# Optimization experiments

Hardware: AMD Instinct MI355X
Metric: run time of the kernel (lower is better)

Reference implementation:

```python
import jax, jax.numpy as jnp
import numpy as np

T, B, H = 256, 512, 2048

def setup_inputs() -> dict:
    key = jax.random.key(0)
    ks = jax.random.split(key, 10)
    s = 1.0 / np.sqrt(H)  # torch RNN/Linear init scale (values only need to be sane)
    return {
        "initial_input": jax.random.normal(ks[0], (B, 1), jnp.float32),
        "hidden": jax.random.normal(ks[1], (B, H), jnp.float32),
        "targets": jax.random.normal(ks[2], (T, B, 1), jnp.float32),
        "W_ih": jax.random.normal(ks[3], (H, 1), jnp.float32) * s,
        "b_ih": jax.random.normal(ks[4], (H,), jnp.float32) * s,
        "W_hh": jax.random.normal(ks[5], (H, H), jnp.float32) * s,
        "b_hh": jax.random.normal(ks[6], (H,), jnp.float32) * s,
        "W_out": jax.random.normal(ks[7], (1, H), jnp.float32) * s,
        "b_out": jax.random.normal(ks[8], (1,), jnp.float32) * s,
        "tf_mask": jax.random.randint(ks[9], (T,), 0, 2) > 0,  # per-step teacher-force decision
    }

def reference(initial_input, hidden, targets, W_ih, b_ih, W_hh, b_hh, W_out, b_out, tf_mask):
    def step(carry, xs):
        h, x = carry                      # h: [B,H], x: [B,1]
        tgt, tf = xs                      # tgt: [B,1], tf: scalar bool
        h = jnp.tanh(x @ W_ih.T + b_ih + h @ W_hh.T + b_hh)  # [B,H]
        y = h @ W_out.T + b_out           # [B,1]
        x_next = jnp.where(tf, tgt, y)
        return (h, x_next), y
    (_, _), outputs = jax.lax.scan(step, (hidden, initial_input), (targets, tf_mask))
    return outputs  # [T,B,1]
```

## Files before the change

kernel.cpp:

```cpp
#include <hip/hip_runtime.h>

using half8   = __attribute__((ext_vector_type(8))) _Float16;
using f32x16  = __attribute__((ext_vector_type(16))) float;
using float4v = __attribute__((ext_vector_type(4))) float;

#define T_STEPS 256
#define BATCH   512
#define HID     2048
#define KS      128

__device__ __forceinline__ f32x16 zero16() {
  f32x16 z;
#pragma unroll
  for (int r = 0; r < 16; ++r) z[r] = 0.0f;
  return z;
}

__device__ __forceinline__ half8 load16_sc0(const half8* p) {
  half8 r;
  asm volatile("global_load_dwordx4 %0, %1, off sc0" : "=v"(r) : "v"(p));
  return r;
}
__device__ __forceinline__ float load4_sc0(const float* p) {
  float r;
  asm volatile("global_load_dword %0, %1, off sc0" : "=v"(r) : "v"(p));
  return r;
}

__global__ void pack_whh_k(const float* __restrict__ whh, half8* __restrict__ bp) {
  int id   = blockIdx.x * 256 + threadIdx.x;
  int lane = id & 63;
  int ks   = (id >> 6) & 127;
  int nblk = id >> 13;
  int j = nblk * 32 + (lane & 31);
  int k = ks * 16 + (lane >> 5) * 8;
  const float4v* src = (const float4v*)(whh + (size_t)j * HID + k);
  float4v a = src[0], b = src[1];
  half8 v;
  v[0]=(_Float16)a[0]; v[1]=(_Float16)a[1]; v[2]=(_Float16)a[2]; v[3]=(_Float16)a[3];
  v[4]=(_Float16)b[0]; v[5]=(_Float16)b[1]; v[6]=(_Float16)b[2]; v[7]=(_Float16)b[3];
  bp[id] = v;
}

__global__ void pack_h_k(const float* __restrict__ hsrc, half8* __restrict__ hp) {
  int id   = blockIdx.x * 256 + threadIdx.x;
  int lane = id & 63;
  int ks   = (id >> 6) & 127;
  int bblk = id >> 13;
  int b = bblk * 32 + (lane & 31);
  int k = ks * 16 + (lane >> 5) * 8;
  const float4v* src = (const float4v*)(hsrc + (size_t)b * HID + k);
  float4v a = src[0], c = src[1];
  half8 v;
  v[0]=(_Float16)a[0]; v[1]=(_Float16)a[1]; v[2]=(_Float16)a[2]; v[3]=(_Float16)a[3];
  v[4]=(_Float16)c[0]; v[5]=(_Float16)c[1]; v[6]=(_Float16)c[2]; v[7]=(_Float16)c[3];
  hp[id] = v;
}

__global__ void bias_k(const float* __restrict__ bih, const float* __restrict__ bhh,
                       float* __restrict__ bias) {
  int i = blockIdx.x * 256 + threadIdx.x;
  if (i < HID) bias[i] = bih[i] + bhh[i];
}

__global__ void tf_expand_k(const int* __restrict__ tf, int* __restrict__ tfc,
                            unsigned* __restrict__ bar) {
  __shared__ int fmt;
  if (threadIdx.x == 0) {
    const unsigned* u = (const unsigned*)tf;
    int all01 = 1;
    for (int i = 0; i < 32; ++i) if (u[i] > 1u) all01 = 0;
    if (all01) {
      int odd0 = 1;
      for (int i = 1; i < 32; i += 2) if (u[i] != 0u) odd0 = 0;
      fmt = odd0 ? 2 : 1;
    } else fmt = 0;
  }
  __syncthreads();
  int i = threadIdx.x;
  int v;
  if (fmt == 2)      v = tf[2 * i];
  else if (fmt == 1) v = tf[i];
  else               v = (int)((const unsigned char*)tf)[i];
  tfc[i] = v ? 1 : 0;
  bar[i] = 0u;
}

__global__ __launch_bounds__(512) void rnn_persist(
    const float* __restrict__ x0,   const float* __restrict__ tgt,
    const int*   __restrict__ tfc,  const float* __restrict__ wih,
    const float* __restrict__ wout, const float* __restrict__ bias,
    const float* __restrict__ bout, const half8* __restrict__ wp,
    half8* __restrict__ h0,         half8* __restrict__ h1,
    float* __restrict__ ypg,        float* __restrict__ out,
    unsigned* __restrict__ bar) {
  __shared__ float part[4][64][68];
  __shared__ float hs[64][68];
  __shared__ float xs[64];
  __shared__ float ypart[8][64];
  __shared__ float wih_s[64], wout_s[64], bias_s[64];
  __shared__ int   tfs[T_STEPS];
  __shared__ int   mn_s[2];

  const int tid = threadIdx.x;
  const int w = tid >> 6;
  const int l = tid & 63;
  const int hi = l >> 5;
  const int c = l & 31;

  if (tid == 0) {
    unsigned xcc = __builtin_amdgcn_s_getreg((31 << 11) | (0 << 6) | 20) & 15u;
    unsigned x = xcc & 7u;
    unsigned r = __hip_atomic_fetch_add(&bar[x * 32 + 16], 1u, __ATOMIC_RELAXED,
                                        __HIP_MEMORY_SCOPE_AGENT);
    mn_s[0] = (int)x;
    mn_s[1] = (int)(r & 31u);
  }
  __syncthreads();
  const int m = mn_s[0];
  const int n = mn_s[1];
  const float bo = bout[0];

  if (tid < 64) {
    int j = n * 64 + tid;
    wih_s[tid]  = wih[j];
    wout_s[tid] = wout[j];
    bias_s[tid] = bias[j];
  }
  if (tid < T_STEPS) tfs[tid] = tfc[tid];

  half8 wb0[16], wb1[16];
  {
    const half8* b0p = wp + ((size_t)(2 * n + 0) * KS + w * 16) * 64 + l;
    const half8* b1p = wp + ((size_t)(2 * n + 1) * KS + w * 16) * 64 + l;
#pragma unroll
    for (int i = 0; i < 16; ++i) { wb0[i] = b0p[i * 64]; wb1[i] = b1p[i * 64]; }
  }
  __syncthreads();

  for (int t = 0; t < T_STEPS; ++t) {
    const half8* hr = (t & 1) ? h1 : h0;
    half8*       hw = (t & 1) ? h0 : h1;

    if (tid < 64) {
      float x;
      if (t == 0) {
        x = x0[m * 64 + tid];
      } else {
        const float* yp = ypg + ((size_t)((t - 1) & 1) * 8 + m) * 32 * 64 + tid;
        float a[32];
#pragma unroll
        for (int i = 0; i < 32; ++i) a[i] = load4_sc0(yp + i * 64);
        asm volatile("s_waitcnt vmcnt(0)" ::: "memory");
        __builtin_amdgcn_sched_barrier(0);
        float s = 0.0f;
#pragma unroll
        for (int i = 0; i < 32; ++i) s += a[i];
        float ysum = s + bo;
        if (n == 0) out[(size_t)(t - 1) * BATCH + m * 64 + tid] = ysum;
        x = tfs[t - 1] ? tgt[(size_t)(t - 1) * BATCH + m * 64 + tid] : ysum;
      }
      xs[tid] = x;
    }

    f32x16 acc00 = zero16(), acc01 = zero16(), acc10 = zero16(), acc11 = zero16();
    {
      const half8* a0p = hr + ((size_t)(2 * m + 0) * KS + w * 16) * 64 + l;
      const half8* a1p = hr + ((size_t)(2 * m + 1) * KS + w * 16) * 64 + l;
#pragma unroll
      for (int kk = 0; kk < 4; ++kk) {
        half8 a0[4], a1[4];
#pragma unroll
        for (int i = 0; i < 4; ++i) {
          a0[i] = load16_sc0(a0p + (kk * 4 + i) * 64);
          a1[i] = load16_sc0(a1p + (kk * 4 + i) * 64);
        }
        asm volatile("s_waitcnt vmcnt(0)" ::: "memory");
        __builtin_amdgcn_sched_barrier(0);
#pragma unroll
        for (int i = 0; i < 4; ++i) {
          acc00 = __builtin_amdgcn_mfma_f32_32x32x16_f16(a0[i], wb0[kk * 4 + i], acc00, 0, 0, 0);
          acc01 = __builtin_amdgcn_mfma_f32_32x32x16_f16(a0[i], wb1[kk * 4 + i], acc01, 0, 0, 0);
          acc10 = __builtin_amdgcn_mfma_f32_32x32x16_f16(a1[i], wb0[kk * 4 + i], acc10, 0, 0, 0);
          acc11 = __builtin_amdgcn_mfma_f32_32x32x16_f16(a1[i], wb1[kk * 4 + i], acc11, 0, 0, 0);
        }
      }
    }

    if (w < 4) {
#pragma unroll
      for (int r = 0; r < 16; ++r) {
        int row0 = (r & 3) + 8 * (r >> 2) + 4 * hi;
        part[w][row0     ][c     ] = acc00[r];
        part[w][row0     ][c + 32] = acc01[r];
        part[w][row0 + 32][c     ] = acc10[r];
        part[w][row0 + 32][c + 32] = acc11[r];
      }
    }
    __syncthreads();
    if (w >= 4) {
      int ww = w - 4;
#pragma unroll
      for (int r = 0; r < 16; ++r) {
        int row0 = (r & 3) + 8 * (r >> 2) + 4 * hi;
        part[ww][row0     ][c     ] += acc00[r];
        part[ww][row0     ][c + 32] += acc01[r];
        part[ww][row0 + 32][c     ] += acc10[r];
        part[ww][row0 + 32][c + 32] += acc11[r];
      }
    }
    __syncthreads();

    {
      int mb = w & 1, nb = (w >> 1) & 1, rh = w >> 2;
#pragma unroll
      for (int r = 0; r < 8; ++r) {
        int rr = rh * 8 + r;
        int row = mb * 32 + (rr & 3) + 8 * (rr >> 2) + 4 * hi;
        int col = nb * 32 + c;
        float s = part[0][row][col] + part[1][row][col]
                + part[2][row][col] + part[3][row][col];
        s += bias_s[col] + xs[row] * wih_s[col];
        hs[row][col] = tanhf(s);
      }
    }
    __syncthreads();

    {
      int row = tid & 63;
      int g   = tid >> 6;
      float hv[8];
      float4v v0 = *(const float4v*)&hs[row][g * 8];
      float4v v1 = *(const float4v*)&hs[row][g * 8 + 4];
      hv[0]=v0[0]; hv[1]=v0[1]; hv[2]=v0[2]; hv[3]=v0[3];
      hv[4]=v1[0]; hv[5]=v1[1]; hv[6]=v1[2]; hv[7]=v1[3];

      float yp = 0.0f;
#pragma unroll
      for (int e = 0; e < 8; ++e) yp += hv[e] * wout_s[g * 8 + e];
      ypart[g][row] = yp;

      half8 f;
#pragma unroll
      for (int e = 0; e < 8; ++e) f[e] = (_Float16)hv[e];
      int bblk = 2 * m + (row >> 5);
      int ksg  = n * 4 + (g >> 1);
      int lane = (g & 1) * 32 + (row & 31);
      hw[((size_t)bblk * KS + ksg) * 64 + lane] = f;
    }
    __syncthreads();

    if (w == 0) {
      float y = ypart[0][tid] + ypart[1][tid] + ypart[2][tid] + ypart[3][tid]
              + ypart[4][tid] + ypart[5][tid] + ypart[6][tid] + ypart[7][tid];
      ypg[(((size_t)(t & 1) * 8 + m) * 32 + n) * 64 + tid] = y;
      asm volatile("s_waitcnt vmcnt(0)" ::: "memory");
    }

    if (tid == 0) {
      __hip_atomic_fetch_add(&bar[m * 32], 1u, __ATOMIC_RELAXED,
                             __HIP_MEMORY_SCOPE_AGENT);
      unsigned tgt_cnt = 32u * (unsigned)(t + 1);
      while (__hip_atomic_load(&bar[m * 32], __ATOMIC_RELAXED,
                               __HIP_MEMORY_SCOPE_AGENT) < tgt_cnt)
        __builtin_amdgcn_s_sleep(1);
    }
    __syncthreads();
  }

  if (n == 0 && tid < 64) {
    const float* yp = ypg + ((size_t)((T_STEPS - 1) & 1) * 8 + m) * 32 * 64 + tid;
    float a[32];
#pragma unroll
    for (int i = 0; i < 32; ++i) a[i] = load4_sc0(yp + i * 64);
    asm volatile("s_waitcnt vmcnt(0)" ::: "memory");
    __builtin_amdgcn_sched_barrier(0);
    float s = 0.0f;
#pragma unroll
    for (int i = 0; i < 32; ++i) s += a[i];
    out[(size_t)(T_STEPS - 1) * BATCH + m * 64 + tid] = s + bo;
  }
}

extern "C" void kernel_launch(void* const* d_in, const int* in_sizes, int n_in,
                              void* d_out, int out_size, void* d_ws, size_t ws_size,
                              hipStream_t stream) {
  (void)in_sizes; (void)n_in; (void)out_size; (void)ws_size;
  const float* x0   = (const float*)d_in[0];
  const float* hid  = (const float*)d_in[1];
  const float* tgt  = (const float*)d_in[2];
  const float* wih  = (const float*)d_in[3];
  const float* bih  = (const float*)d_in[4];
  const float* whh  = (const float*)d_in[5];
  const float* bhh  = (const float*)d_in[6];
  const float* wout = (const float*)d_in[7];
  const float* bout = (const float*)d_in[8];
  const int*   tf   = (const int*)d_in[9];
  float* out = (float*)d_out;

  char* ws = (char*)d_ws;
  half8*    wp   = (half8*)ws;
  half8*    h0   = (half8*)(ws + (8u  << 20));
  half8*    h1   = (half8*)(ws + (10u << 20));
  float*    bias = (float*)(ws + (12u << 20));
  int*      tfc  = (int*)  (ws + (12u << 20) + 8192);
  unsigned* bar  = (unsigned*)(ws + (12u << 20) + 16384);
  float*    ypg  = (float*)(ws + (12u << 20) + 32768);

  pack_whh_k <<<2048, 256, 0, stream>>>(whh, wp);
  pack_h_k   <<<512,  256, 0, stream>>>(hid, h0);
  bias_k     <<<8,    256, 0, stream>>>(bih, bhh, bias);
  tf_expand_k<<<1,    256, 0, stream>>>(tf, tfc, bar);

  rnn_persist<<<256, 512, 0, stream>>>(x0, tgt, tfc, wih, wout, bias, bout,
                                       wp, h0, h1, ypg, out, bar);
}
```

Baseline: 2.128 ms.

## Use system-coherent loads/stores, static block mapping, and fast tanh

Cross-block exchange loads and stores of h and partial outputs now carry sc0 sc1 instead of sc0 only, so data is shared through a farther coherence level instead of relying on same-XCD L2 placement. Block-to-(m,n) mapping now comes straight from blockIdx instead of the XCC-id plus atomic-counter assignment. tanhf is replaced by a formula built on __expf. The goal is to drop the startup atomic and the slower tanh, but each step's exchange may now pay higher load/store latency, and the fast tanh changes precision slightly.

```diff
diff --git a/kernel.cpp b/kernel.cpp
--- a/kernel.cpp
+++ b/kernel.cpp
@@ -16,15 +16,21 @@
   return z;
 }
 
-__device__ __forceinline__ half8 load16_sc0(const half8* p) {
+__device__ __forceinline__ half8 load16_llc(const half8* p) {
   half8 r;
-  asm volatile("global_load_dwordx4 %0, %1, off sc0" : "=v"(r) : "v"(p));
+  asm volatile("global_load_dwordx4 %0, %1, off sc0 sc1" : "=v"(r) : "v"(p));
   return r;
 }
-__device__ __forceinline__ float load4_sc0(const float* p) {
+__device__ __forceinline__ float loadf_llc(const float* p) {
   float r;
-  asm volatile("global_load_dword %0, %1, off sc0" : "=v"(r) : "v"(p));
+  asm volatile("global_load_dword %0, %1, off sc0 sc1" : "=v"(r) : "v"(p));
   return r;
+}
+__device__ __forceinline__ void store16_llc(half8* p, half8 v) {
+  asm volatile("global_store_dwordx4 %0, %1, off sc0 sc1" :: "v"(p), "v"(v) : "memory");
+}
+__device__ __forceinline__ void storef_llc(float* p, float v) {
+  asm volatile("global_store_dword %0, %1, off sc0 sc1" :: "v"(p), "v"(v) : "memory");
 }
 
 __global__ void pack_whh_k(const float* __restrict__ whh, half8* __restrict__ bp) {
@@ -100,25 +106,16 @@
   __shared__ float ypart[8][64];
   __shared__ float wih_s[64], wout_s[64], bias_s[64];
   __shared__ int   tfs[T_STEPS];
-  __shared__ int   mn_s[2];
-
+
+  const int bid = blockIdx.x;
+  const int m = bid & 7;
+  const int n = bid >> 3;
   const int tid = threadIdx.x;
   const int w = tid >> 6;
   const int l = tid & 63;
   const int hi = l >> 5;
   const int c = l & 31;
 
-  if (tid == 0) {
-    unsigned xcc = __builtin_amdgcn_s_getreg((31 << 11) | (0 << 6) | 20) & 15u;
-    unsigned x = xcc & 7u;
-    unsigned r = __hip_atomic_fetch_add(&bar[x * 32 + 16], 1u, __ATOMIC_RELAXED,
-                                        __HIP_MEMORY_SCOPE_AGENT);
-    mn_s[0] = (int)x;
-    mn_s[1] = (int)(r & 31u);
-  }
-  __syncthreads();
-  const int m = mn_s[0];
-  const int n = mn_s[1];
   const float bo = bout[0];
 
   if (tid < 64) {
@@ -147,10 +144,10 @@
       if (t == 0) {
         x = x0[m * 64 + tid];
       } else {
-        const float* yp = ypg + ((size_t)((t - 1) & 1) * 8 + m) * 32 * 64 + tid;
+        const float* yp = ypg + ((size_t)((t - 1) & 1) * 8 + m) * 2048 + tid;
         float a[32];
 #pragma unroll
-        for (int i = 0; i < 32; ++i) a[i] = load4_sc0(yp + i * 64);
+        for (int i = 0; i < 32; ++i) a[i] = loadf_llc(yp + i * 64);
         asm volatile("s_waitcnt vmcnt(0)" ::: "memory");
         __builtin_amdgcn_sched_barrier(0);
         float s = 0.0f;
@@ -172,8 +169,8 @@
         half8 a0[4], a1[4];
 #pragma unroll
         for (int i = 0; i < 4; ++i) {
-          a0[i] = load16_sc0(a0p + (kk * 4 + i) * 64);
-          a1[i] = load16_sc0(a1p + (kk * 4 + i) * 64);
+          a0[i] = load16_llc(a0p + (kk * 4 + i) * 64);
+          a1[i] = load16_llc(a1p + (kk * 4 + i) * 64);
         }
         asm volatile("s_waitcnt vmcnt(0)" ::: "memory");
         __builtin_amdgcn_sched_barrier(0);
@@ -221,7 +218,8 @@
         float s = part[0][row][col] + part[1][row][col]
                 + part[2][row][col] + part[3][row][col];
         s += bias_s[col] + xs[row] * wih_s[col];
-        hs[row][col] = tanhf(s);
+        float e = __expf(2.0f * s);
+        hs[row][col] = 1.0f - 2.0f / (e + 1.0f);
       }
     }
     __syncthreads();
@@ -246,14 +244,14 @@
       int bblk = 2 * m + (row >> 5);
       int ksg  = n * 4 + (g >> 1);
       int lane = (g & 1) * 32 + (row & 31);
-      hw[((size_t)bblk * KS + ksg) * 64 + lane] = f;
+      store16_llc(hw + ((size_t)bblk * KS + ksg) * 64 + lane, f);
     }
     __syncthreads();
 
     if (w == 0) {
-      float y = ypart[0][tid] + ypart[1][tid] + ypart[2][tid] + ypart[3][tid]
-              + ypart[4][tid] + ypart[5][tid] + ypart[6][tid] + ypart[7][tid];
-      ypg[(((size_t)(t & 1) * 8 + m) * 32 + n) * 64 + tid] = y;
+      float y = ypart[0][l] + ypart[1][l] + ypart[2][l] + ypart[3][l]
+              + ypart[4][l] + ypart[5][l] + ypart[6][l] + ypart[7][l];
+      storef_llc(ypg + (((size_t)(t & 1) * 8 + m) * 32 + n) * 64 + l, y);
       asm volatile("s_waitcnt vmcnt(0)" ::: "memory");
     }
 
@@ -269,10 +267,10 @@
   }
 
   if (n == 0 && tid < 64) {
-    const float* yp = ypg + ((size_t)((T_STEPS - 1) & 1) * 8 + m) * 32 * 64 + tid;
+    const float* yp = ypg + ((size_t)((T_STEPS - 1) & 1) * 8 + m) * 2048 + tid;
     float a[32];
 #pragma unroll
-    for (int i = 0; i < 32; ++i) a[i] = load4_sc0(yp + i * 64);
+    for (int i = 0; i < 32; ++i) a[i] = loadf_llc(yp + i * 64);
     asm volatile("s_waitcnt vmcnt(0)" ::: "memory");
     __builtin_amdgcn_sched_barrier(0);
     float s = 0.0f;
```

After: 2.036 ms. 4.3% less time.
